# Kernel optimization log

Hardware: AMD Instinct MI355X
Metric: run time of the kernel (lower is better)

The kernel has to match this reference:

```python
import jax, jax.numpy as jnp
import numpy as np

S, B = 64, 16          # seq_len, batch
V = 32000              # ntoken
NINP = 512             # ninp (embedding / decoder input dim)
NHID = 1536            # nhid (intermediate LSTM layers)
NHL = 1024             # nhidlast (last LSTM layer)
E = 8                  # n_experts


def setup_inputs() -> dict:
    key = jax.random.key(0)
    ks = jax.random.split(key, 24)

    def unif(k, shape, r=0.1):
        return jax.random.uniform(k, shape, jnp.float32, -r, r)

    inp = {
        "tokens": jax.random.randint(ks[0], (S, B), 0, V),
        "h0": jnp.zeros((B, NHID), jnp.float32),
        "c0": jnp.zeros((B, NHID), jnp.float32),
        "h1": jnp.zeros((B, NHID), jnp.float32),
        "c1": jnp.zeros((B, NHID), jnp.float32),
        "h2": jnp.zeros((B, NHL), jnp.float32),
        "c2": jnp.zeros((B, NHL), jnp.float32),
        # parameters
        "emb": unif(ks[1], (V, NINP)),
        "Wih0": unif(ks[2], (4 * NHID, NINP)),
        "Whh0": unif(ks[3], (4 * NHID, NHID)),
        "b0": jnp.zeros((4 * NHID,), jnp.float32),
        "Wih1": unif(ks[4], (4 * NHID, NHID)),
        "Whh1": unif(ks[5], (4 * NHID, NHID)),
        "b1": jnp.zeros((4 * NHID,), jnp.float32),
        "Wih2": unif(ks[6], (4 * NHL, NHID)),
        "Whh2": unif(ks[7], (4 * NHL, NHL)),
        "b2": jnp.zeros((4 * NHL,), jnp.float32),
        "prior_W": unif(ks[8], (E, NHL)),
        "latent_W": unif(ks[9], (E * NINP, NHL)),
        "latent_b": jnp.zeros((E * NINP,), jnp.float32),
        "dec_W": unif(ks[10], (V, NINP)),
        "dec_b": jnp.zeros((V,), jnp.float32),
        "gain": jnp.ones((NINP,), jnp.float32),   # decoder_gain (frozen ones)
    }
    return inp


def _lstm_layer(x, h0, c0, Wih, Whh, b):
    # x: (S, B, Din); gate order i, f, g, o as in torch
    xg = jnp.einsum('sbd,gd->sbg', x, Wih) + b  # precompute input projections

    def step(carry, xt):
        h, c = carry
        g = xt + h @ Whh.T
        i, f, gg, o = jnp.split(g, 4, axis=-1)
        c = jax.nn.sigmoid(f) * c + jax.nn.sigmoid(i) * jnp.tanh(gg)
        h = jax.nn.sigmoid(o) * jnp.tanh(c)
        return (h, c), h

    (hT, cT), ys = jax.lax.scan(step, (h0, c0), xg)
    return ys, hT, cT


def reference(tokens, h0, c0, h1, c1, h2, c2, emb, Wih0, Whh0, b0,
              Wih1, Whh1, b1, Wih2, Whh2, b2, prior_W, latent_W, latent_b,
              dec_W, dec_b, gain):
    x = emb[tokens]                                   # (S, B, NINP)
    x, _, _ = _lstm_layer(x, h0, c0, Wih0, Whh0, b0)  # (S, B, NHID)
    x, _, _ = _lstm_layer(x, h1, c1, Wih1, Whh1, b1)  # (S, B, NHID)
    out, _, _ = _lstm_layer(x, h2, c2, Wih2, Whh2, b2)  # (S, B, NHL)

    # MoS head
    latent = jnp.tanh(jnp.einsum('sbh,eh->sbe', out, latent_W) + latent_b)
    latent = latent.reshape(S * B * E, NINP)          # (S*B*E, NINP)
    logit = (latent * gain) @ dec_W.T + dec_b         # (S*B*E, V)
    prior = jax.nn.softmax(out.reshape(S * B, NHL) @ prior_W.T, axis=-1)  # (S*B, E)
    prob = jax.nn.softmax(logit, axis=-1).reshape(S * B, E, V)
    prob = jnp.einsum('nev,ne->nv', prob, prior)      # mixture over experts
    log_prob = jnp.log(prob + 1e-8)
    return log_prob.reshape(S, B, V)
```

## Files before the change

kernel.cpp:

```cpp
#include <hip/hip_runtime.h>
#include <hip/hip_bf16.h>

typedef __attribute__((ext_vector_type(8))) short short8;
typedef __attribute__((ext_vector_type(4))) float f32x4;
typedef unsigned short u16;
typedef unsigned long long u64;

__device__ __forceinline__ u16 f2b(float f) {
    unsigned u = __float_as_uint(f);
    return (u16)((u + 0x7FFFu + ((u >> 16) & 1u)) >> 16);
}
__device__ __forceinline__ float b2f(u16 u) {
    return __uint_as_float(((unsigned)u) << 16);
}
__device__ __forceinline__ void gload16(const void* g, void* l) {
    __builtin_amdgcn_global_load_lds(
        (const __attribute__((address_space(1))) void*)g,
        (__attribute__((address_space(3))) void*)l, 16, 0, 0);
}

__global__ __launch_bounds__(256)
void k_f2b(const float* __restrict__ s, u16* __restrict__ d, int n4)
{
    int i = blockIdx.x * 256 + threadIdx.x;
    if (i >= n4) return;
    float4 v = ((const float4*)s)[i];
    short4 o;
    o.x = (short)f2b(v.x); o.y = (short)f2b(v.y);
    o.z = (short)f2b(v.z); o.w = (short)f2b(v.w);
    ((short4*)d)[i] = o;
}

__global__ __launch_bounds__(256)
void k_embed(const int* __restrict__ tok, const float* __restrict__ emb,
             u16* __restrict__ x0)
{
    int i = blockIdx.x * 256 + threadIdx.x;
    int n = i >> 7, p4 = i & 127;
    float4 v = ((const float4*)(emb + (size_t)tok[n] * 512))[p4];
    short4 o;
    o.x = (short)f2b(v.x); o.y = (short)f2b(v.y);
    o.z = (short)f2b(v.z); o.w = (short)f2b(v.w);
    ((short4*)x0)[i] = o;
}

template <int EPI, int BIN>
__global__ __launch_bounds__(256)
void k_gemm(const u16* __restrict__ A, const void* __restrict__ Bp,
            const float* __restrict__ bias, void* __restrict__ Cp,
            int M, int N, int K, const float* __restrict__ gain,
            float* __restrict__ rsum)
{
    __shared__ __align__(16) u16 As[128 * 32];
    __shared__ __align__(16) u16 Bs[128 * 32];
    __shared__ float rs[2][128];
    const int tid = threadIdx.x;
    const int lane = tid & 63, wid = tid >> 6;
    const int wr = wid >> 1, wc = wid & 1;
    const int l15 = lane & 15, l4 = lane >> 4;
    const int row0 = blockIdx.y * 128, col0 = blockIdx.x * 128;

    const int srA = wid * 16 + (lane >> 2);
    const int skA = (lane & 3) * 8;
    const int srow = tid >> 1, skh = (tid & 1) << 4;

    f32x4 acc[4][4] = {};

    for (int k0 = 0; k0 < K; k0 += 32) {
        if (k0) __syncthreads();
        gload16(A + (size_t)(row0 + srA) * K + k0 + skA, As + wid * 512);
        gload16(A + (size_t)(row0 + 64 + srA) * K + k0 + skA, As + 2048 + wid * 512);
        if (BIN == 1) {
            const u16* B = (const u16*)Bp;
            gload16(B + (size_t)(col0 + srA) * K + k0 + skA, Bs + wid * 512);
            gload16(B + (size_t)(col0 + 64 + srA) * K + k0 + skA, Bs + 2048 + wid * 512);
        } else {
            const float* B = (const float*)Bp;
            const float4* sb = (const float4*)(B + (size_t)(col0 + srow) * K + k0 + skh);
            float tmp[16];
            *(float4*)&tmp[0]  = sb[0];
            *(float4*)&tmp[4]  = sb[1];
            *(float4*)&tmp[8]  = sb[2];
            *(float4*)&tmp[12] = sb[3];
            short8 v0, v1;
#pragma unroll
            for (int i = 0; i < 8; ++i) { v0[i] = (short)f2b(tmp[i]); v1[i] = (short)f2b(tmp[8 + i]); }
            *(short8*)&Bs[srow * 32 + skh]     = v0;
            *(short8*)&Bs[srow * 32 + skh + 8] = v1;
        }
        __syncthreads();

        short8 af[4], bfv[4];
#pragma unroll
        for (int i = 0; i < 4; ++i)
            af[i]  = *(const short8*)&As[(wr * 64 + i * 16 + l15) * 32 + l4 * 8];
#pragma unroll
        for (int i = 0; i < 4; ++i)
            bfv[i] = *(const short8*)&Bs[(wc * 64 + i * 16 + l15) * 32 + l4 * 8];
#pragma unroll
        for (int mi = 0; mi < 4; ++mi)
#pragma unroll
            for (int ni = 0; ni < 4; ++ni)
                acc[mi][ni] = __builtin_amdgcn_mfma_f32_16x16x32_bf16(
                    af[mi], bfv[ni], acc[mi][ni], 0, 0, 0);
    }

    if (EPI == 2) {
#pragma unroll
        for (int mi = 0; mi < 4; ++mi) {
#pragma unroll
            for (int j = 0; j < 4; ++j) {
                int rb = row0 + wr * 64 + mi * 16 + l4 * 4 + j;
                float rsub = 0.f;
#pragma unroll
                for (int ni = 0; ni < 4; ++ni) {
                    int cc = col0 + wc * 64 + ni * 16 + l15;
                    float pv = expf(fminf(acc[mi][ni][j] + bias[cc], 80.f));
                    ((u16*)Cp)[(size_t)rb * N + cc] = f2b(pv);
                    rsub += pv;
                }
#pragma unroll
                for (int o = 1; o < 16; o <<= 1) rsub += __shfl_xor(rsub, o, 64);
                if (l15 == 0)
                    rs[wc][wr * 64 + mi * 16 + l4 * 4 + j] = rsub;
            }
        }
        __syncthreads();
        if (tid < 128)
            atomicAdd(&rsum[row0 + tid], rs[0][tid] + rs[1][tid]);
        return;
    }

#pragma unroll
    for (int mi = 0; mi < 4; ++mi) {
#pragma unroll
        for (int ni = 0; ni < 4; ++ni) {
            int rb = row0 + wr * 64 + mi * 16 + l4 * 4;
            int cc = col0 + wc * 64 + ni * 16 + l15;
            float bv = bias[cc];
#pragma unroll
            for (int j = 0; j < 4; ++j) {
                float v = acc[mi][ni][j] + bv;
                if (EPI == 0) {
                    ((float*)Cp)[(size_t)(rb + j) * N + cc] = v;
                } else {
                    int e = cc >> 9, pp = cc & 511;
                    ((u16*)Cp)[(((size_t)(rb + j) * 8 + e) << 9) | pp] =
                        f2b(tanhf(v) * gain[pp]);
                }
            }
        }
    }
}

__global__ __launch_bounds__(512)
void k_gemm_dec(const u16* __restrict__ A, const u16* __restrict__ B,
                const float* __restrict__ bias, u16* __restrict__ pe,
                int M, int N, int K, float* __restrict__ rsum)
{
    __shared__ __align__(16) u16 As[256 * 32];
    __shared__ __align__(16) u16 Bs[128 * 32];
    __shared__ float rs[2][256];
    const int tid = threadIdx.x;
    const int lane = tid & 63, wid = tid >> 6;
    const int wr = wid >> 1, wc = wid & 1;
    const int l15 = lane & 15, l4 = lane >> 4;
    const int row0 = blockIdx.y * 256, col0 = blockIdx.x * 128;

    const int srA = wid * 16 + (lane >> 2);
    const int skA = (lane & 3) * 8;

    f32x4 acc[4][4] = {};

    for (int k0 = 0; k0 < K; k0 += 32) {
        if (k0) __syncthreads();
        gload16(A + (size_t)(row0 + srA) * K + k0 + skA, As + wid * 512);
        gload16(A + (size_t)(row0 + 128 + srA) * K + k0 + skA, As + 4096 + wid * 512);
        gload16(B + (size_t)(col0 + srA) * K + k0 + skA, Bs + wid * 512);
        __syncthreads();

        short8 af[4], bfv[4];
#pragma unroll
        for (int i = 0; i < 4; ++i)
            af[i]  = *(const short8*)&As[(wr * 64 + i * 16 + l15) * 32 + l4 * 8];
#pragma unroll
        for (int i = 0; i < 4; ++i)
            bfv[i] = *(const short8*)&Bs[(wc * 64 + i * 16 + l15) * 32 + l4 * 8];
#pragma unroll
        for (int mi = 0; mi < 4; ++mi)
#pragma unroll
            for (int ni = 0; ni < 4; ++ni)
                acc[mi][ni] = __builtin_amdgcn_mfma_f32_16x16x32_bf16(
                    af[mi], bfv[ni], acc[mi][ni], 0, 0, 0);
    }

#pragma unroll
    for (int mi = 0; mi < 4; ++mi) {
#pragma unroll
        for (int j = 0; j < 4; ++j) {
            int rloc = wr * 64 + mi * 16 + l4 * 4 + j;
            float rsub = 0.f;
#pragma unroll
            for (int ni = 0; ni < 4; ++ni) {
                int cc = col0 + wc * 64 + ni * 16 + l15;
                float pv = expf(fminf(acc[mi][ni][j] + bias[cc], 80.f));
                pe[(size_t)(row0 + rloc) * N + cc] = f2b(pv);
                rsub += pv;
            }
#pragma unroll
            for (int o = 1; o < 16; o <<= 1) rsub += __shfl_xor(rsub, o, 64);
            if (l15 == 0) rs[wc][rloc] = rsub;
        }
    }
    __syncthreads();
    if (tid < 256)
        atomicAdd(&rsum[row0 + tid], rs[0][tid] + rs[1][tid]);
}

template <int DH>
__global__ void __launch_bounds__(512)
k_rnn(const float* __restrict__ xg,
      const u16* __restrict__ W,
      const float* __restrict__ h0f,
      const float* __restrict__ c0f,
      u16* __restrict__ y,
      unsigned* __restrict__ bar,
      int nb)
{
    constexpr int DH2 = DH / 2;
    constexpr int NSH = DH2 / 32;
    constexpr int NL  = 16 * DH / 4 / 512;
    constexpr int RW  = DH / 4;
    constexpr int LDH = DH + 8;
    __shared__ __align__(16) u16 hs[16][LDH];
    __shared__ __align__(16) f32x4 red[8][64];
    __shared__ __align__(16) u16 hout[16][16];

    const int tid = threadIdx.x;
    const int lane = tid & 63, wid = tid >> 6;
    const int g = wid & 3, kh = wid >> 2;
    const int l15 = lane & 15, l4 = lane >> 4;
    const int u0 = blockIdx.x * 16;

    short8 wfr[NSH];
    {
        const u16* wa = W + (size_t)(g * DH + u0 + l15) * DH + kh * DH2 + l4 * 8;
#pragma unroll
        for (int s = 0; s < NSH; ++s) wfr[s] = *(const short8*)(wa + s * 32);
    }

    const int eb = tid >> 4, eu = tid & 15;
    float c_reg = (tid < 256) ? c0f[(size_t)eb * DH + u0 + eu] : 0.f;

    for (int t = 0; t < 64; ++t) {
        float xpre[4];
        if (tid < 256) {
            const float* xr = xg + (size_t)(t * 16 + eb) * 4 * DH + u0 + eu;
#pragma unroll
            for (int gg = 0; gg < 4; ++gg) xpre[gg] = xr[(size_t)gg * DH];
        }

        if (t == 0) {
            for (int i = tid; i < 16 * DH / 4; i += 512) {
                int r = i / (DH / 4), k4 = i % (DH / 4);
                float4 v = *(const float4*)(h0f + (size_t)r * DH + k4 * 4);
                short4 o;
                o.x = (short)f2b(v.x); o.y = (short)f2b(v.y);
                o.z = (short)f2b(v.z); o.w = (short)f2b(v.w);
                *(short4*)&hs[r][k4 * 4] = o;
            }
            __syncthreads();
        } else {
            if (tid < nb) {
                while (__hip_atomic_load(bar + tid * 32, __ATOMIC_RELAXED,
                                         __HIP_MEMORY_SCOPE_AGENT) < (unsigned)t)
                    __builtin_amdgcn_s_sleep(1);
            }
            __syncthreads();
            const u64* hp = (const u64*)(y + (size_t)(t - 1) * 16 * DH);
            u64 tmp[NL];
#pragma unroll
            for (int j = 0; j < NL; ++j)
                tmp[j] = __hip_atomic_load(hp + tid + j * 512, __ATOMIC_RELAXED,
                                           __HIP_MEMORY_SCOPE_AGENT);
#pragma unroll
            for (int j = 0; j < NL; ++j) {
                int idx = tid + j * 512;
                int r = idx / RW, c = (idx % RW) * 4;
                *(u64*)&hs[r][c] = tmp[j];
            }
            __syncthreads();
        }

        f32x4 acc = {};
#pragma unroll
        for (int s = 0; s < NSH; ++s) {
            short8 hf = *(const short8*)&hs[l15][kh * DH2 + s * 32 + l4 * 8];
            acc = __builtin_amdgcn_mfma_f32_16x16x32_bf16(hf, wfr[s], acc, 0, 0, 0);
        }
        red[wid][lane] = acc;
        __syncthreads();

        if (tid < 256) {
            const int li = (eb >> 2) * 16 + eu, j = eb & 3;
            float gt[4];
#pragma unroll
            for (int gg = 0; gg < 4; ++gg)
                gt[gg] = ((const float*)&red[gg][li])[j]
                       + ((const float*)&red[4 + gg][li])[j]
                       + xpre[gg];
            float si = 1.f / (1.f + expf(-gt[0]));
            float sf = 1.f / (1.f + expf(-gt[1]));
            float so = 1.f / (1.f + expf(-gt[3]));
            c_reg = sf * c_reg + si * tanhf(gt[2]);
            hout[eb][eu] = f2b(so * tanhf(c_reg));
        }
        __syncthreads();

        if (tid < 64) {
            int r = tid >> 2, c4 = (tid & 3) * 4;
            u64 v = *(const u64*)&hout[r][c4];
            __hip_atomic_store((u64*)(y + (size_t)(t * 16 + r) * DH + u0 + c4), v,
                               __ATOMIC_RELAXED, __HIP_MEMORY_SCOPE_AGENT);
        }

        if (t < 63) {
            __syncthreads();
            if (tid == 0)
                __hip_atomic_store(bar + blockIdx.x * 32, (unsigned)(t + 1),
                                   __ATOMIC_RELAXED, __HIP_MEMORY_SCOPE_AGENT);
        }
    }
}

__global__ __launch_bounds__(256)
void k_prior(const u16* __restrict__ out2, const float* __restrict__ pW,
             float* __restrict__ prior)
{
    const int n = blockIdx.x;
    const int tid = threadIdx.x;
    const int e = tid >> 5, lane = tid & 31;
    const u16* x = out2 + (size_t)n * 1024;
    const float* w = pW + (size_t)e * 1024;
    float s = 0.f;
    for (int k = lane; k < 1024; k += 32) s += b2f(x[k]) * w[k];
#pragma unroll
    for (int o = 16; o; o >>= 1) s += __shfl_down(s, o, 32);
    __shared__ float es[8];
    if (lane == 0) es[e] = s;
    __syncthreads();
    if (tid == 0) {
        float m = -1e30f;
        for (int i = 0; i < 8; ++i) m = fmaxf(m, es[i]);
        float Z = 0.f, ex[8];
        for (int i = 0; i < 8; ++i) { ex[i] = expf(es[i] - m); Z += ex[i]; }
        for (int i = 0; i < 8; ++i) prior[(size_t)n * 8 + i] = ex[i] / Z;
    }
}

__global__ __launch_bounds__(256)
void k_combine(const u16* __restrict__ pe, const float* __restrict__ prior,
               const float* __restrict__ rsum, float* __restrict__ out, int n0)
{
    const int v = blockIdx.x * 256 + threadIdx.x;
    const int nl = blockIdx.y;
    __shared__ float w[8];
    if (threadIdx.x < 8)
        w[threadIdx.x] = prior[(size_t)(n0 + nl) * 8 + threadIdx.x]
                       / rsum[nl * 8 + threadIdx.x];
    __syncthreads();
    float acc = 0.f;
#pragma unroll
    for (int e = 0; e < 8; ++e)
        acc += b2f(pe[(size_t)(nl * 8 + e) * 32000 + v]) * w[e];
    out[(size_t)(n0 + nl) * 32000 + v] = logf(acc + 1e-8f);
}

extern "C" void kernel_launch(void* const* d_in, const int* in_sizes, int n_in,
                              void* d_out, int out_size, void* d_ws, size_t ws_size,
                              hipStream_t stream)
{
    const int*   tok  = (const int*)d_in[0];
    const float* h0   = (const float*)d_in[1];
    const float* c0   = (const float*)d_in[2];
    const float* h1   = (const float*)d_in[3];
    const float* c1   = (const float*)d_in[4];
    const float* h2   = (const float*)d_in[5];
    const float* c2   = (const float*)d_in[6];
    const float* emb  = (const float*)d_in[7];
    const float* Wih0 = (const float*)d_in[8];
    const float* Whh0 = (const float*)d_in[9];
    const float* b0   = (const float*)d_in[10];
    const float* Wih1 = (const float*)d_in[11];
    const float* Whh1 = (const float*)d_in[12];
    const float* b1   = (const float*)d_in[13];
    const float* Wih2 = (const float*)d_in[14];
    const float* Whh2 = (const float*)d_in[15];
    const float* b2   = (const float*)d_in[16];
    const float* priW = (const float*)d_in[17];
    const float* latW = (const float*)d_in[18];
    const float* latb = (const float*)d_in[19];
    const float* decW = (const float*)d_in[20];
    const float* decb = (const float*)d_in[21];
    const float* gain = (const float*)d_in[22];

    char* p = (char*)d_ws;
    auto alloc = [&](size_t bytes) {
        char* r = p; p += (bytes + 255) & ~(size_t)255; return r;
    };
    u16* Whh0b = (u16*)alloc(6144ull * 1536 * 2);
    u16* Whh1b = (u16*)alloc(6144ull * 1536 * 2);
    u16* Whh2b = (u16*)alloc(4096ull * 1024 * 2);
    u16* latWb = (u16*)alloc(4096ull * 1024 * 2);
    u16* decWb = (u16*)alloc(32000ull * 512 * 2);
    u16* latb16 = (u16*)alloc(8192ull * 512 * 2);
    float* pri   = (float*)alloc(8192 * 4);
    float* rowsum = (float*)alloc(8192 * 4);
    u16* out2 = (u16*)alloc(1024ull * 1024 * 2);
    unsigned* bars = (unsigned*)alloc(3 * 96 * 32 * 4);
    char* trans = p;
    u16* x0 = (u16*)alloc(1024ull * 512 * 2);
    u16* x1 = (u16*)alloc(1024ull * 1536 * 2);
    u16* x2 = (u16*)alloc(1024ull * 1536 * 2);
    float* xg = (float*)alloc(1024ull * 6144 * 4);
    u16* pe = (u16*)trans;
    size_t cap = ws_size - (size_t)(trans - (char*)d_ws);
    int chunkRows = 128;
    if (cap >= 1024ull * 32000 * 2) chunkRows = 1024;
    else if (cap >= 512ull * 32000 * 2) chunkRows = 512;
    else if (cap >= 256ull * 32000 * 2) chunkRows = 256;
    int nPer = chunkRows / 8;

    hipMemsetAsync(bars, 0, 3 * 96 * 32 * 4, stream);
    hipMemsetAsync(rowsum, 0, 8192 * 4, stream);

    k_f2b<<<9216, 256, 0, stream>>>(Whh0, Whh0b, 2359296);
    k_f2b<<<9216, 256, 0, stream>>>(Whh1, Whh1b, 2359296);
    k_f2b<<<4096, 256, 0, stream>>>(Whh2, Whh2b, 1048576);
    k_f2b<<<4096, 256, 0, stream>>>(latW, latWb, 1048576);
    k_f2b<<<16000, 256, 0, stream>>>(decW, decWb, 4096000);
    k_embed<<<512, 256, 0, stream>>>(tok, emb, x0);

    k_gemm<0, 0><<<dim3(48, 8), 256, 0, stream>>>(
        x0, Wih0, b0, xg, 1024, 6144, 512, nullptr, nullptr);
    {
        unsigned* bar = bars;
        int nb = 96;
        void* args[] = {(void*)&xg, (void*)&Whh0b, (void*)&h0, (void*)&c0,
                        (void*)&x1, (void*)&bar, (void*)&nb};
        hipLaunchCooperativeKernel(reinterpret_cast<void*>(&k_rnn<1536>),
                                   dim3(96), dim3(512), args, 0, stream);
    }

    k_gemm<0, 0><<<dim3(48, 8), 256, 0, stream>>>(
        x1, Wih1, b1, xg, 1024, 6144, 1536, nullptr, nullptr);
    {
        unsigned* bar = bars + 96 * 32;
        int nb = 96;
        void* args[] = {(void*)&xg, (void*)&Whh1b, (void*)&h1, (void*)&c1,
                        (void*)&x2, (void*)&bar, (void*)&nb};
        hipLaunchCooperativeKernel(reinterpret_cast<void*>(&k_rnn<1536>),
                                   dim3(96), dim3(512), args, 0, stream);
    }

    k_gemm<0, 0><<<dim3(32, 8), 256, 0, stream>>>(
        x2, Wih2, b2, xg, 1024, 4096, 1536, nullptr, nullptr);
    {
        unsigned* bar = bars + 2 * 96 * 32;
        int nb = 64;
        void* args[] = {(void*)&xg, (void*)&Whh2b, (void*)&h2, (void*)&c2,
                        (void*)&out2, (void*)&bar, (void*)&nb};
        hipLaunchCooperativeKernel(reinterpret_cast<void*>(&k_rnn<1024>),
                                   dim3(64), dim3(512), args, 0, stream);
    }

    k_prior<<<1024, 256, 0, stream>>>(out2, priW, pri);
    k_gemm<1, 1><<<dim3(32, 8), 256, 0, stream>>>(
        out2, latWb, latb, latb16, 1024, 4096, 1024, gain, nullptr);

    for (int nb = 0; nb < 1024; nb += nPer) {
        const u16* Ach = latb16 + (size_t)nb * 8 * 512;
        float* rsumc = rowsum + (size_t)nb * 8;
        if (chunkRows >= 256) {
            k_gemm_dec<<<dim3(250, chunkRows / 256), 512, 0, stream>>>(
                Ach, decWb, decb, pe, chunkRows, 32000, 512, rsumc);
        } else {
            k_gemm<2, 1><<<dim3(250, chunkRows / 128), 256, 0, stream>>>(
                Ach, decWb, decb, pe, chunkRows, 32000, 512, nullptr, rsumc);
        }
        k_combine<<<dim3(125, nPer), 256, 0, stream>>>(
            pe, pri, rowsum + nb * 8, (float*)d_out, nb);
    }
}
```

Baseline: 1.531 ms.

## Enlarge decoder GEMM tile, vectorize combine, pre-convert input weights to bf16

The decoder GEMM now uses a 256x256 tile with 8 waves, each holding 8x4 MFMA accumulators, so fewer blocks reload the A panel. k_combine handles two vocab entries per thread, using 32-bit bf16 pair loads and float2 stores. The Wih weight matrices are converted to bf16 up front, and the input-projection GEMMs use the bf16 B-operand path. The trade-offs are higher register pressure in the decoder kernel and extra conversion launches.

```diff
diff --git a/kernel.cpp b/kernel.cpp
--- a/kernel.cpp
+++ b/kernel.cpp
@@ -154,40 +154,41 @@
 }
 
 __global__ __launch_bounds__(512)
-void k_gemm_dec(const u16* __restrict__ A, const u16* __restrict__ B,
-                const float* __restrict__ bias, u16* __restrict__ pe,
-                int M, int N, int K, float* __restrict__ rsum)
+void k_gemm_dec2(const u16* __restrict__ A, const u16* __restrict__ B,
+                 const float* __restrict__ bias, u16* __restrict__ pe,
+                 int M, int N, int K, float* __restrict__ rsum)
 {
     __shared__ __align__(16) u16 As[256 * 32];
-    __shared__ __align__(16) u16 Bs[128 * 32];
-    __shared__ float rs[2][256];
+    __shared__ __align__(16) u16 Bs[256 * 32];
+    __shared__ float rs[4][256];
     const int tid = threadIdx.x;
     const int lane = tid & 63, wid = tid >> 6;
-    const int wr = wid >> 1, wc = wid & 1;
+    const int wr = wid >> 2, wc = wid & 3;
     const int l15 = lane & 15, l4 = lane >> 4;
-    const int row0 = blockIdx.y * 256, col0 = blockIdx.x * 128;
+    const int row0 = blockIdx.y * 256, col0 = blockIdx.x * 256;
 
     const int srA = wid * 16 + (lane >> 2);
     const int skA = (lane & 3) * 8;
 
-    f32x4 acc[4][4] = {};
+    f32x4 acc[8][4] = {};
 
     for (int k0 = 0; k0 < K; k0 += 32) {
         if (k0) __syncthreads();
         gload16(A + (size_t)(row0 + srA) * K + k0 + skA, As + wid * 512);
         gload16(A + (size_t)(row0 + 128 + srA) * K + k0 + skA, As + 4096 + wid * 512);
         gload16(B + (size_t)(col0 + srA) * K + k0 + skA, Bs + wid * 512);
+        gload16(B + (size_t)(col0 + 128 + srA) * K + k0 + skA, Bs + 4096 + wid * 512);
         __syncthreads();
 
-        short8 af[4], bfv[4];
-#pragma unroll
-        for (int i = 0; i < 4; ++i)
-            af[i]  = *(const short8*)&As[(wr * 64 + i * 16 + l15) * 32 + l4 * 8];
+        short8 af[8], bfv[4];
+#pragma unroll
+        for (int i = 0; i < 8; ++i)
+            af[i]  = *(const short8*)&As[(wr * 128 + i * 16 + l15) * 32 + l4 * 8];
 #pragma unroll
         for (int i = 0; i < 4; ++i)
             bfv[i] = *(const short8*)&Bs[(wc * 64 + i * 16 + l15) * 32 + l4 * 8];
 #pragma unroll
-        for (int mi = 0; mi < 4; ++mi)
+        for (int mi = 0; mi < 8; ++mi)
 #pragma unroll
             for (int ni = 0; ni < 4; ++ni)
                 acc[mi][ni] = __builtin_amdgcn_mfma_f32_16x16x32_bf16(
@@ -195,10 +196,10 @@
     }
 
 #pragma unroll
-    for (int mi = 0; mi < 4; ++mi) {
+    for (int mi = 0; mi < 8; ++mi) {
 #pragma unroll
         for (int j = 0; j < 4; ++j) {
-            int rloc = wr * 64 + mi * 16 + l4 * 4 + j;
+            int rloc = wr * 128 + mi * 16 + l4 * 4 + j;
             float rsub = 0.f;
 #pragma unroll
             for (int ni = 0; ni < 4; ++ni) {
@@ -214,7 +215,8 @@
     }
     __syncthreads();
     if (tid < 256)
-        atomicAdd(&rsum[row0 + tid], rs[0][tid] + rs[1][tid]);
+        atomicAdd(&rsum[row0 + tid],
+                  rs[0][tid] + rs[1][tid] + rs[2][tid] + rs[3][tid]);
 }
 
 template <int DH>
@@ -358,22 +360,28 @@
     }
 }
 
-__global__ __launch_bounds__(256)
+__global__ __launch_bounds__(128)
 void k_combine(const u16* __restrict__ pe, const float* __restrict__ prior,
                const float* __restrict__ rsum, float* __restrict__ out, int n0)
 {
-    const int v = blockIdx.x * 256 + threadIdx.x;
+    const int v2 = blockIdx.x * 128 + threadIdx.x;
     const int nl = blockIdx.y;
     __shared__ float w[8];
     if (threadIdx.x < 8)
         w[threadIdx.x] = prior[(size_t)(n0 + nl) * 8 + threadIdx.x]
                        / rsum[nl * 8 + threadIdx.x];
     __syncthreads();
-    float acc = 0.f;
-#pragma unroll
-    for (int e = 0; e < 8; ++e)
-        acc += b2f(pe[(size_t)(nl * 8 + e) * 32000 + v]) * w[e];
-    out[(size_t)(n0 + nl) * 32000 + v] = logf(acc + 1e-8f);
+    float a0 = 0.f, a1 = 0.f;
+#pragma unroll
+    for (int e = 0; e < 8; ++e) {
+        unsigned pv = *(const unsigned*)&pe[(size_t)(nl * 8 + e) * 32000 + v2 * 2];
+        a0 += b2f((u16)(pv & 0xffff)) * w[e];
+        a1 += b2f((u16)(pv >> 16)) * w[e];
+    }
+    float2 o;
+    o.x = logf(a0 + 1e-8f);
+    o.y = logf(a1 + 1e-8f);
+    *(float2*)&out[(size_t)(n0 + nl) * 32000 + v2 * 2] = o;
 }
 
 extern "C" void kernel_launch(void* const* d_in, const int* in_sizes, int n_in,
@@ -419,6 +427,9 @@
     u16* out2 = (u16*)alloc(1024ull * 1024 * 2);
     unsigned* bars = (unsigned*)alloc(3 * 96 * 32 * 4);
     char* trans = p;
+    u16* Wih0b = (u16*)alloc(6144ull * 512 * 2);
+    u16* Wih1b = (u16*)alloc(6144ull * 1536 * 2);
+    u16* Wih2b = (u16*)alloc(4096ull * 1536 * 2);
     u16* x0 = (u16*)alloc(1024ull * 512 * 2);
     u16* x1 = (u16*)alloc(1024ull * 1536 * 2);
     u16* x2 = (u16*)alloc(1024ull * 1536 * 2);
@@ -437,12 +448,15 @@
     k_f2b<<<9216, 256, 0, stream>>>(Whh0, Whh0b, 2359296);
     k_f2b<<<9216, 256, 0, stream>>>(Whh1, Whh1b, 2359296);
     k_f2b<<<4096, 256, 0, stream>>>(Whh2, Whh2b, 1048576);
+    k_f2b<<<3072, 256, 0, stream>>>(Wih0, Wih0b, 786432);
+    k_f2b<<<9216, 256, 0, stream>>>(Wih1, Wih1b, 2359296);
+    k_f2b<<<6144, 256, 0, stream>>>(Wih2, Wih2b, 1572864);
     k_f2b<<<4096, 256, 0, stream>>>(latW, latWb, 1048576);
     k_f2b<<<16000, 256, 0, stream>>>(decW, decWb, 4096000);
     k_embed<<<512, 256, 0, stream>>>(tok, emb, x0);
 
-    k_gemm<0, 0><<<dim3(48, 8), 256, 0, stream>>>(
-        x0, Wih0, b0, xg, 1024, 6144, 512, nullptr, nullptr);
+    k_gemm<0, 1><<<dim3(48, 8), 256, 0, stream>>>(
+        x0, Wih0b, b0, xg, 1024, 6144, 512, nullptr, nullptr);
     {
         unsigned* bar = bars;
         int nb = 96;
@@ -452,8 +466,8 @@
                                    dim3(96), dim3(512), args, 0, stream);
     }
 
-    k_gemm<0, 0><<<dim3(48, 8), 256, 0, stream>>>(
-        x1, Wih1, b1, xg, 1024, 6144, 1536, nullptr, nullptr);
+    k_gemm<0, 1><<<dim3(48, 8), 256, 0, stream>>>(
+        x1, Wih1b, b1, xg, 1024, 6144, 1536, nullptr, nullptr);
     {
         unsigned* bar = bars + 96 * 32;
         int nb = 96;
@@ -463,8 +477,8 @@
                                    dim3(96), dim3(512), args, 0, stream);
     }
 
-    k_gemm<0, 0><<<dim3(32, 8), 256, 0, stream>>>(
-        x2, Wih2, b2, xg, 1024, 4096, 1536, nullptr, nullptr);
+    k_gemm<0, 1><<<dim3(32, 8), 256, 0, stream>>>(
+        x2, Wih2b, b2, xg, 1024, 4096, 1536, nullptr, nullptr);
     {
         unsigned* bar = bars + 2 * 96 * 32;
         int nb = 64;
@@ -482,13 +496,13 @@
         const u16* Ach = latb16 + (size_t)nb * 8 * 512;
         float* rsumc = rowsum + (size_t)nb * 8;
         if (chunkRows >= 256) {
-            k_gemm_dec<<<dim3(250, chunkRows / 256), 512, 0, stream>>>(
+            k_gemm_dec2<<<dim3(125, chunkRows / 256), 512, 0, stream>>>(
                 Ach, decWb, decb, pe, chunkRows, 32000, 512, rsumc);
         } else {
             k_gemm<2, 1><<<dim3(250, chunkRows / 128), 256, 0, stream>>>(
                 Ach, decWb, decb, pe, chunkRows, 32000, 512, nullptr, rsumc);
         }
-        k_combine<<<dim3(125, nPer), 256, 0, stream>>>(
+        k_combine<<<dim3(125, nPer), 128, 0, stream>>>(
             pe, pri, rowsum + nb * 8, (float*)d_out, nb);
     }
 }
```

New measurement: 1.560 ms. About the same (+1.9%).
